# Kernel tuning notes

Hardware: AMD Instinct MI355X
Metric: run time of the kernel (lower is better)

The kernel has to match this reference:

```python
import jax, jax.numpy as jnp
import numpy as np

# Dimensions
B, T, S, V, CV, D = 32, 128, 400, 32000, 600, 512
PAD = 1  # vocabs['code'].stoi['<blank>']


def setup_inputs() -> dict:
    key = jax.random.key(0)
    k0, k1, k2, k3, k4 = jax.random.split(key, 5)
    hidden = jax.random.normal(k0, (B * T, D), dtype=jnp.float32)
    # attention weights: normalized over source length
    copy_attn = jax.nn.softmax(jax.random.normal(k1, (B * T, S), dtype=jnp.float32), axis=-1)
    # src_map: one-hot scatter matrix [B, S, CV] mapping src positions to extended-vocab ids
    src_ids = jax.random.randint(k2, (B, S), 0, CV)
    src_map = jax.nn.one_hot(src_ids, CV, dtype=jnp.float32)
    W = jax.random.normal(k3, (V, D), dtype=jnp.float32) * 0.02
    b = jnp.zeros((V,), dtype=jnp.float32)
    w_copy = jax.random.normal(k4, (D,), dtype=jnp.float32) * 0.02
    b_copy = jnp.zeros((), dtype=jnp.float32)
    return {"hidden": hidden, "copy_attn": copy_attn, "src_map": src_map,
            "W": W, "b": b, "w_copy": w_copy, "b_copy": b_copy}


def reference(hidden, copy_attn, src_map, W, b, w_copy, b_copy):
    # logits over target vocab, pad logit masked to -inf
    logits = hidden @ W.T + b                      # [B*T, V]
    logits = logits.at[:, PAD].set(-jnp.inf)
    prob = jax.nn.softmax(logits, axis=-1)         # [B*T, V]
    # copy gate p(z)
    copy = jax.nn.sigmoid(hidden @ w_copy + b_copy)[:, None]  # [B*T, 1]
    out_prob = prob * (1.0 - copy)                 # generation branch
    mul_attn = copy_attn * copy                    # copy branch, [B*T, S]
    # scatter attention mass into extended vocab via one-hot bmm
    copy_prob = jnp.einsum('bts,bsv->btv', mul_attn.reshape(B, T, S), src_map)
    copy_prob = copy_prob.reshape(-1, src_map.shape[-1])  # [B*T, CV]
    return jnp.concatenate([out_prob, copy_prob], axis=1)  # [B*T, V+CV]
```

## Files before the change

kernel.cpp:

```cpp
#include <hip/hip_runtime.h>
#include <hip/hip_bf16.h>
#include <hip/hip_fp8.h>
#include <cstdint>
#include <cstddef>

#define M_ROWS   4096
#define N_VOCAB  32000
#define K_DIM    512
#define S_DIM    400
#define CV_DIM   600
#define OUT_PITCH 32600
#define PAD_IDX  1

typedef __attribute__((ext_vector_type(8))) short short8;
typedef __attribute__((ext_vector_type(8))) unsigned short ushort8;
typedef __attribute__((ext_vector_type(4))) float f32x4;
typedef long long i64;

#define W8_OFF   0ull
#define H8_OFF   16384000ull
#define COPYG_OFF 18481152ull
#define RSUM_OFF  18497536ull
#define SSCALE_OFF 18513920ull
#define SRCID_OFF 18530304ull
#define EB_OFF    18581504ull
#define WS_NEED   (EB_OFF + 262144000ull)

__device__ inline void gload_lds16(const void* g, void* l) {
  __builtin_amdgcn_global_load_lds(
      (const __attribute__((address_space(1))) unsigned int*)g,
      (__attribute__((address_space(3))) unsigned int*)l, 16, 0, 0);
}

__device__ inline unsigned short f32_to_bf16_rn(float f) {
  unsigned u = __float_as_uint(f);
  u += 0x7FFFu + ((u >> 16) & 1u);
  return (unsigned short)(u >> 16);
}
__device__ inline float bf16_to_f32(unsigned short h) {
  return __uint_as_float((unsigned)h << 16);
}
__device__ inline unsigned f32_to_fp8(float f) {
  __hip_fp8_e4m3 q(f);
  return (unsigned)(unsigned char)q.__x;
}

__global__ void cvt8_kernel(const float4* __restrict__ in, unsigned* __restrict__ out, unsigned n4) {
  unsigned stride = gridDim.x * blockDim.x;
  for (unsigned i = blockIdx.x * blockDim.x + threadIdx.x; i < n4; i += stride) {
    float4 v = in[i];
    out[i] = f32_to_fp8(v.x) | (f32_to_fp8(v.y) << 8)
           | (f32_to_fp8(v.z) << 16) | (f32_to_fp8(v.w) << 24);
  }
}

__global__ void copygate_cvt_kernel(const float* __restrict__ hidden,
                                    const float* __restrict__ w_copy,
                                    const float* __restrict__ b_copy,
                                    float* __restrict__ copyg,
                                    unsigned char* __restrict__ H8) {
  unsigned gw = (blockIdx.x * blockDim.x + threadIdx.x) >> 6;
  unsigned lane = threadIdx.x & 63u;
  if (gw >= M_ROWS) return;
  const float4* h4 = (const float4*)(hidden + (size_t)gw * K_DIM);
  const float4* w4 = (const float4*)w_copy;
  float4 a0 = h4[lane * 2 + 0], w0 = w4[lane * 2 + 0];
  float4 a1 = h4[lane * 2 + 1], w1 = w4[lane * 2 + 1];
  float dot = a0.x * w0.x + a0.y * w0.y + a0.z * w0.z + a0.w * w0.w
            + a1.x * w1.x + a1.y * w1.y + a1.z * w1.z + a1.w * w1.w;
  unsigned lo = f32_to_fp8(a0.x) | (f32_to_fp8(a0.y) << 8)
              | (f32_to_fp8(a0.z) << 16) | (f32_to_fp8(a0.w) << 24);
  unsigned hi = f32_to_fp8(a1.x) | (f32_to_fp8(a1.y) << 8)
              | (f32_to_fp8(a1.z) << 16) | (f32_to_fp8(a1.w) << 24);
  uint2 pk; pk.x = lo; pk.y = hi;
  *(uint2*)(H8 + (size_t)gw * K_DIM + lane * 8u) = pk;
  #pragma unroll
  for (int mask = 1; mask < 64; mask <<= 1) dot += __shfl_xor(dot, mask);
  if (lane == 0) copyg[gw] = 1.f / (1.f + __expf(-(dot + b_copy[0])));
}

__global__ void srcids_kernel(const float* __restrict__ src_map, int* __restrict__ src_ids) {
  unsigned pos = (blockIdx.x * blockDim.x + threadIdx.x) >> 6;
  unsigned lane = threadIdx.x & 63u;
  if (pos >= 32 * S_DIM) return;
  const float* row = src_map + (size_t)pos * CV_DIM;
  int found = 1 << 30;
  for (int v = lane; v < CV_DIM; v += 64)
    if (row[v] > 0.5f) found = v;
  #pragma unroll
  for (int mask = 1; mask < 64; mask <<= 1) {
    int o = __shfl_xor(found, mask);
    found = found < o ? found : o;
  }
  if (lane == 0) src_ids[pos] = found;
}

template<int BF16OUT>
__global__ __launch_bounds__(512, 2)
void gemm_exp_kernel(const unsigned char* __restrict__ A,
                     const unsigned char* __restrict__ B,
                     const float* __restrict__ bias,
                     float* __restrict__ out,
                     unsigned short* __restrict__ Eb,
                     float* __restrict__ row_sum) {
  __shared__ unsigned char smem[49152];
  unsigned char* As = smem;
  unsigned char* Bs = smem + 32768;

  unsigned bid = blockIdx.x;
  unsigned xcd = bid & 7u, local = bid >> 3;
  unsigned slab = xcd >> 1, half = xcd & 1u;
  unsigned nt = half * 125u + (local >> 2);
  unsigned mt = slab * 4u + (local & 3u);
  unsigned m0 = mt * 256u, n0 = nt * 128u;

  unsigned tid = threadIdx.x;
  unsigned lane = tid & 63u;
  unsigned wid = tid >> 6;
  unsigned wm = wid >> 1, wn = wid & 1u;
  unsigned lr = lane >> 4, lc = lane & 15u;

  const unsigned char* Asrc[4];
  const unsigned char* Bsrc[2];
  unsigned dstA[4], dstB[2];
  #pragma unroll
  for (unsigned i = 0; i < 4; ++i) {
    unsigned u = i * 512u + tid;
    unsigned rr = u >> 3;
    unsigned ch = (u & 7u) ^ (rr & 7u);
    dstA[i] = u * 16u;
    Asrc[i] = A + (size_t)(m0 + rr) * K_DIM + ch * 16u;
  }
  #pragma unroll
  for (unsigned i = 0; i < 2; ++i) {
    unsigned u = i * 512u + tid;
    unsigned rr = u >> 3;
    unsigned ch = (u & 7u) ^ (rr & 7u);
    dstB[i] = u * 16u;
    Bsrc[i] = B + (size_t)(n0 + rr) * K_DIM + ch * 16u;
  }
  unsigned abase[4], akey[4], bbase[4], bkey[4];
  #pragma unroll
  for (int m = 0; m < 4; ++m) {
    unsigned r = wm * 64u + m * 16u + lc;
    abase[m] = r * 128u; akey[m] = r & 7u;
  }
  #pragma unroll
  for (int n = 0; n < 4; ++n) {
    unsigned r = wn * 64u + n * 16u + lc;
    bbase[n] = r * 128u; bkey[n] = r & 7u;
  }
  const unsigned hsel = (lr & 1u) * 8u;

  f32x4 acc[4][4] = {};

  for (unsigned kt = 0; kt < 4; ++kt) {
    unsigned k0 = kt * 128u;
    #pragma unroll
    for (unsigned i = 0; i < 4; ++i)
      gload_lds16(Asrc[i] + k0, As + dstA[i]);
    #pragma unroll
    for (unsigned i = 0; i < 2; ++i)
      gload_lds16(Bsrc[i] + k0, Bs + dstB[i]);
    __syncthreads();
    #pragma unroll
    for (unsigned ks = 0; ks < 4; ++ks) {
      unsigned h = ks * 2u + (lr >> 1);
      i64 av[4], bv[4];
      #pragma unroll
      for (int m = 0; m < 4; ++m)
        av[m] = *(const i64*)(As + abase[m] + ((h ^ akey[m]) * 16u) + hsel);
      #pragma unroll
      for (int n = 0; n < 4; ++n)
        bv[n] = *(const i64*)(Bs + bbase[n] + ((h ^ bkey[n]) * 16u) + hsel);
      #pragma unroll
      for (int m = 0; m < 4; ++m)
        #pragma unroll
        for (int n = 0; n < 4; ++n)
          acc[m][n] = __builtin_amdgcn_mfma_f32_16x16x32_fp8_fp8(bv[n], av[m],
                                                                 acc[m][n], 0, 0, 0);
    }
    __syncthreads();
  }

  float4 bv4[4];
  #pragma unroll
  for (int n = 0; n < 4; ++n)
    bv4[n] = *(const float4*)&bias[n0 + wn * 64u + n * 16u + lr * 4u];

  if (BF16OUT) {
    #pragma unroll
    for (int m = 0; m < 4; ++m) {
      unsigned grow = m0 + wm * 64u + m * 16u + lc;
      unsigned short* rowp = Eb + (size_t)grow * N_VOCAB;
      #pragma unroll
      for (int n = 0; n < 4; ++n) {
        unsigned gcol = n0 + wn * 64u + n * 16u + lr * 4u;
        float e0 = (gcol + 0u == PAD_IDX) ? 0.f : __expf(acc[m][n][0] + bv4[n].x);
        float e1 = (gcol + 1u == PAD_IDX) ? 0.f : __expf(acc[m][n][1] + bv4[n].y);
        float e2 = (gcol + 2u == PAD_IDX) ? 0.f : __expf(acc[m][n][2] + bv4[n].z);
        float e3 = (gcol + 3u == PAD_IDX) ? 0.f : __expf(acc[m][n][3] + bv4[n].w);
        ushort4 o;
        o.x = f32_to_bf16_rn(e0); o.y = f32_to_bf16_rn(e1);
        o.z = f32_to_bf16_rn(e2); o.w = f32_to_bf16_rn(e3);
        *(ushort4*)(rowp + gcol) = o;
      }
    }
  } else {
    #pragma unroll
    for (int m = 0; m < 4; ++m) {
      unsigned grow = m0 + wm * 64u + m * 16u + lc;
      float rs = 0.f;
      #pragma unroll
      for (int n = 0; n < 4; ++n) {
        unsigned gcol = n0 + wn * 64u + n * 16u + lr * 4u;
        float4 e;
        e.x = (gcol + 0u == PAD_IDX) ? 0.f : __expf(acc[m][n][0] + bv4[n].x);
        e.y = (gcol + 1u == PAD_IDX) ? 0.f : __expf(acc[m][n][1] + bv4[n].y);
        e.z = (gcol + 2u == PAD_IDX) ? 0.f : __expf(acc[m][n][2] + bv4[n].z);
        e.w = (gcol + 3u == PAD_IDX) ? 0.f : __expf(acc[m][n][3] + bv4[n].w);
        *(float4*)(out + (size_t)grow * OUT_PITCH + gcol) = e;
        rs += e.x + e.y + e.z + e.w;
      }
      rs += __shfl_xor(rs, 16);
      rs += __shfl_xor(rs, 32);
      if (lr == 0) atomicAdd(&row_sum[grow], rs);
    }
  }
}

__global__ __launch_bounds__(256)
void norm_scale_kernel(const unsigned short* __restrict__ Eb,
                       const float* __restrict__ copyg,
                       float* __restrict__ out) {
  unsigned r = blockIdx.x;
  unsigned tid = threadIdx.x;
  const ushort8* src = (const ushort8*)(Eb + (size_t)r * N_VOCAB);
  ushort8 v[16];
  float lsum = 0.f;
  #pragma unroll
  for (int i = 0; i < 16; ++i) {
    unsigned c = (unsigned)i * 256u + tid;
    if (c < 4000u) {
      v[i] = src[c];
      #pragma unroll
      for (int k = 0; k < 8; ++k) lsum += bf16_to_f32(v[i][k]);
    }
  }
  #pragma unroll
  for (int mask = 1; mask < 64; mask <<= 1) lsum += __shfl_xor(lsum, mask);
  __shared__ float wsum[4];
  if ((tid & 63u) == 0) wsum[tid >> 6] = lsum;
  __syncthreads();
  float s = (1.f - copyg[r]) / (wsum[0] + wsum[1] + wsum[2] + wsum[3]);
  float* dst = out + (size_t)r * OUT_PITCH;
  #pragma unroll
  for (int i = 0; i < 16; ++i) {
    unsigned c = (unsigned)i * 256u + tid;
    if (c < 4000u) {
      float4 lo, hi;
      lo.x = bf16_to_f32(v[i][0]) * s; lo.y = bf16_to_f32(v[i][1]) * s;
      lo.z = bf16_to_f32(v[i][2]) * s; lo.w = bf16_to_f32(v[i][3]) * s;
      hi.x = bf16_to_f32(v[i][4]) * s; hi.y = bf16_to_f32(v[i][5]) * s;
      hi.z = bf16_to_f32(v[i][6]) * s; hi.w = bf16_to_f32(v[i][7]) * s;
      float4* o = (float4*)(dst + c * 8u);
      o[0] = lo; o[1] = hi;
    }
  }
}

__global__ void finalize_kernel(const float* __restrict__ row_sum, const float* __restrict__ copyg,
                                float* __restrict__ sscale) {
  unsigned r = blockIdx.x * blockDim.x + threadIdx.x;
  if (r < M_ROWS) sscale[r] = (1.f - copyg[r]) / row_sum[r];
}

__global__ void scale_kernel(float4* __restrict__ out, const float* __restrict__ sscale) {
  const unsigned total = M_ROWS * (N_VOCAB / 4);
  unsigned stride = gridDim.x * blockDim.x;
  for (unsigned i = blockIdx.x * blockDim.x + threadIdx.x; i < total; i += stride) {
    unsigned r = i / (N_VOCAB / 4);
    unsigned c = i % (N_VOCAB / 4);
    float s = sscale[r];
    float4 v = out[(size_t)r * (OUT_PITCH / 4) + c];
    v.x *= s; v.y *= s; v.z *= s; v.w *= s;
    out[(size_t)r * (OUT_PITCH / 4) + c] = v;
  }
}

__global__ void copyprob_kernel(const float* __restrict__ attn, const int* __restrict__ src_ids,
                                const float* __restrict__ copyg, float* __restrict__ out) {
  unsigned r = blockIdx.x;
  unsigned tid = threadIdx.x;
  __shared__ float cp[CV_DIM];
  for (unsigned v = tid; v < CV_DIM; v += 128) cp[v] = 0.f;
  __syncthreads();
  unsigned batch = r >> 7;
  float g = copyg[r];
  for (unsigned s = tid; s < S_DIM; s += 128) {
    float a = attn[(size_t)r * S_DIM + s] * g;
    atomicAdd(&cp[src_ids[batch * S_DIM + s]], a);
  }
  __syncthreads();
  for (unsigned v = tid; v < CV_DIM; v += 128)
    out[(size_t)r * OUT_PITCH + N_VOCAB + v] = cp[v];
}

extern "C" void kernel_launch(void* const* d_in, const int* in_sizes, int n_in,
                              void* d_out, int out_size, void* d_ws, size_t ws_size,
                              hipStream_t stream) {
  const float* hidden    = (const float*)d_in[0];
  const float* copy_attn = (const float*)d_in[1];
  const float* src_map   = (const float*)d_in[2];
  const float* W         = (const float*)d_in[3];
  const float* bias      = (const float*)d_in[4];
  const float* w_copy    = (const float*)d_in[5];
  const float* b_copy    = (const float*)d_in[6];
  float* out = (float*)d_out;

  char* ws = (char*)d_ws;
  unsigned char* W8 = (unsigned char*)(ws + W8_OFF);
  unsigned char* H8 = (unsigned char*)(ws + H8_OFF);
  float* copyg   = (float*)(ws + COPYG_OFF);
  float* row_sum = (float*)(ws + RSUM_OFF);
  float* sscale  = (float*)(ws + SSCALE_OFF);
  int*   src_ids = (int*)(ws + SRCID_OFF);
  unsigned short* Eb = (unsigned short*)(ws + EB_OFF);

  const bool bf16_path = (ws_size >= WS_NEED);

  cvt8_kernel<<<2048, 256, 0, stream>>>((const float4*)W, (unsigned*)W8,
                                        (unsigned)(N_VOCAB * K_DIM / 4));
  copygate_cvt_kernel<<<M_ROWS / 4, 256, 0, stream>>>(hidden, w_copy, b_copy, copyg, H8);
  srcids_kernel<<<(32 * S_DIM) / 4, 256, 0, stream>>>(src_map, src_ids);

  if (bf16_path) {
    gemm_exp_kernel<1><<<(M_ROWS / 256) * (N_VOCAB / 128), 512, 0, stream>>>(
        H8, W8, bias, out, Eb, row_sum);
    norm_scale_kernel<<<M_ROWS, 256, 0, stream>>>(Eb, copyg, out);
  } else {
    hipMemsetAsync(row_sum, 0, M_ROWS * sizeof(float), stream);
    gemm_exp_kernel<0><<<(M_ROWS / 256) * (N_VOCAB / 128), 512, 0, stream>>>(
        H8, W8, bias, out, Eb, row_sum);
    finalize_kernel<<<(M_ROWS + 255) / 256, 256, 0, stream>>>(row_sum, copyg, sscale);
    scale_kernel<<<4096, 256, 0, stream>>>((float4*)out, sscale);
  }

  copyprob_kernel<<<M_ROWS, 128, 0, stream>>>(copy_attn, src_ids, copyg, out);
}
```

Measured before the change: 363.5 us.

## Double-buffer GEMM K-tiles and fuse copy-prob scatter into normalize kernel

The fp8 GEMM now uses 64-wide K tiles in two LDS buffers and prefetches the next tile while computing the current one, aiming to hide global-load latency. The copy-probability scatter is folded into the normalize/scale kernel using shared-memory atomics, removing a separate launch on the bf16 path. Smaller K tiles mean more iterations and barriers, and the synchronization around buffer reuse must be correct to avoid races.

```diff
diff --git a/kernel.cpp b/kernel.cpp
--- a/kernel.cpp
+++ b/kernel.cpp
@@ -104,8 +104,6 @@
                      unsigned short* __restrict__ Eb,
                      float* __restrict__ row_sum) {
   __shared__ unsigned char smem[49152];
-  unsigned char* As = smem;
-  unsigned char* Bs = smem + 32768;
 
   unsigned bid = blockIdx.x;
   unsigned xcd = bid & 7u, local = bid >> 3;
@@ -120,59 +118,67 @@
   unsigned wm = wid >> 1, wn = wid & 1u;
   unsigned lr = lane >> 4, lc = lane & 15u;
 
-  const unsigned char* Asrc[4];
-  const unsigned char* Bsrc[2];
-  unsigned dstA[4], dstB[2];
-  #pragma unroll
-  for (unsigned i = 0; i < 4; ++i) {
+  const unsigned char* Asrc[2];
+  const unsigned char* Bsrc0;
+  unsigned dstA[2], dstB0;
+  #pragma unroll
+  for (unsigned i = 0; i < 2; ++i) {
     unsigned u = i * 512u + tid;
-    unsigned rr = u >> 3;
-    unsigned ch = (u & 7u) ^ (rr & 7u);
+    unsigned rr = u >> 2;
+    unsigned ch = (u & 3u) ^ (rr & 3u);
     dstA[i] = u * 16u;
     Asrc[i] = A + (size_t)(m0 + rr) * K_DIM + ch * 16u;
   }
-  #pragma unroll
-  for (unsigned i = 0; i < 2; ++i) {
-    unsigned u = i * 512u + tid;
-    unsigned rr = u >> 3;
-    unsigned ch = (u & 7u) ^ (rr & 7u);
-    dstB[i] = u * 16u;
-    Bsrc[i] = B + (size_t)(n0 + rr) * K_DIM + ch * 16u;
+  {
+    unsigned u = tid;
+    unsigned rr = u >> 2;
+    unsigned ch = (u & 3u) ^ (rr & 3u);
+    dstB0 = u * 16u;
+    Bsrc0 = B + (size_t)(n0 + rr) * K_DIM + ch * 16u;
   }
   unsigned abase[4], akey[4], bbase[4], bkey[4];
   #pragma unroll
   for (int m = 0; m < 4; ++m) {
     unsigned r = wm * 64u + m * 16u + lc;
-    abase[m] = r * 128u; akey[m] = r & 7u;
+    abase[m] = r * 64u; akey[m] = r & 3u;
   }
   #pragma unroll
   for (int n = 0; n < 4; ++n) {
     unsigned r = wn * 64u + n * 16u + lc;
-    bbase[n] = r * 128u; bkey[n] = r & 7u;
+    bbase[n] = 16384u + r * 64u; bkey[n] = r & 3u;
   }
   const unsigned hsel = (lr & 1u) * 8u;
 
   f32x4 acc[4][4] = {};
 
-  for (unsigned kt = 0; kt < 4; ++kt) {
-    unsigned k0 = kt * 128u;
+  {
+    unsigned char* base = smem;
+    gload_lds16(Asrc[0], base + dstA[0]);
+    gload_lds16(Asrc[1], base + dstA[1]);
+    gload_lds16(Bsrc0, base + 16384u + dstB0);
+  }
+  __syncthreads();
+
+  for (unsigned kt = 0; kt < 8; ++kt) {
+    unsigned buf = kt & 1u;
+    if (kt < 7) {
+      unsigned k0 = (kt + 1u) * 64u;
+      unsigned char* base = smem + (buf ^ 1u) * 24576u;
+      gload_lds16(Asrc[0] + k0, base + dstA[0]);
+      gload_lds16(Asrc[1] + k0, base + dstA[1]);
+      gload_lds16(Bsrc0 + k0, base + 16384u + dstB0);
+    }
+    const unsigned char* cbase = smem + buf * 24576u;
     #pragma unroll
-    for (unsigned i = 0; i < 4; ++i)
-      gload_lds16(Asrc[i] + k0, As + dstA[i]);
-    #pragma unroll
-    for (unsigned i = 0; i < 2; ++i)
-      gload_lds16(Bsrc[i] + k0, Bs + dstB[i]);
-    __syncthreads();
-    #pragma unroll
-    for (unsigned ks = 0; ks < 4; ++ks) {
+    for (unsigned ks = 0; ks < 2; ++ks) {
       unsigned h = ks * 2u + (lr >> 1);
       i64 av[4], bv[4];
       #pragma unroll
       for (int m = 0; m < 4; ++m)
-        av[m] = *(const i64*)(As + abase[m] + ((h ^ akey[m]) * 16u) + hsel);
+        av[m] = *(const i64*)(cbase + abase[m] + ((h ^ akey[m]) * 16u) + hsel);
       #pragma unroll
       for (int n = 0; n < 4; ++n)
-        bv[n] = *(const i64*)(Bs + bbase[n] + ((h ^ bkey[n]) * 16u) + hsel);
+        bv[n] = *(const i64*)(cbase + bbase[n] + ((h ^ bkey[n]) * 16u) + hsel);
       #pragma unroll
       for (int m = 0; m < 4; ++m)
         #pragma unroll
@@ -230,11 +236,17 @@
 }
 
 __global__ __launch_bounds__(256)
-void norm_scale_kernel(const unsigned short* __restrict__ Eb,
-                       const float* __restrict__ copyg,
-                       float* __restrict__ out) {
+void norm_scale_copy_kernel(const unsigned short* __restrict__ Eb,
+                            const float* __restrict__ copyg,
+                            const float* __restrict__ attn,
+                            const int* __restrict__ src_ids,
+                            float* __restrict__ out) {
   unsigned r = blockIdx.x;
   unsigned tid = threadIdx.x;
+  __shared__ float cp[CV_DIM];
+  __shared__ float wsum[4];
+  for (unsigned v2 = tid; v2 < CV_DIM; v2 += 256) cp[v2] = 0.f;
+
   const ushort8* src = (const ushort8*)(Eb + (size_t)r * N_VOCAB);
   ushort8 v[16];
   float lsum = 0.f;
@@ -249,10 +261,18 @@
   }
   #pragma unroll
   for (int mask = 1; mask < 64; mask <<= 1) lsum += __shfl_xor(lsum, mask);
-  __shared__ float wsum[4];
   if ((tid & 63u) == 0) wsum[tid >> 6] = lsum;
   __syncthreads();
-  float s = (1.f - copyg[r]) / (wsum[0] + wsum[1] + wsum[2] + wsum[3]);
+
+  float g = copyg[r];
+  float s = (1.f - g) / (wsum[0] + wsum[1] + wsum[2] + wsum[3]);
+
+  unsigned batch = r >> 7;
+  for (unsigned sp = tid; sp < S_DIM; sp += 256) {
+    float a = attn[(size_t)r * S_DIM + sp] * g;
+    atomicAdd(&cp[src_ids[batch * S_DIM + sp]], a);
+  }
+
   float* dst = out + (size_t)r * OUT_PITCH;
   #pragma unroll
   for (int i = 0; i < 16; ++i) {
@@ -267,6 +287,9 @@
       o[0] = lo; o[1] = hi;
     }
   }
+  __syncthreads();
+  for (unsigned v2 = tid; v2 < CV_DIM; v2 += 256)
+    dst[N_VOCAB + v2] = cp[v2];
 }
 
 __global__ void finalize_kernel(const float* __restrict__ row_sum, const float* __restrict__ copyg,
@@ -337,14 +360,13 @@
   if (bf16_path) {
     gemm_exp_kernel<1><<<(M_ROWS / 256) * (N_VOCAB / 128), 512, 0, stream>>>(
         H8, W8, bias, out, Eb, row_sum);
-    norm_scale_kernel<<<M_ROWS, 256, 0, stream>>>(Eb, copyg, out);
+    norm_scale_copy_kernel<<<M_ROWS, 256, 0, stream>>>(Eb, copyg, copy_attn, src_ids, out);
   } else {
     hipMemsetAsync(row_sum, 0, M_ROWS * sizeof(float), stream);
     gemm_exp_kernel<0><<<(M_ROWS / 256) * (N_VOCAB / 128), 512, 0, stream>>>(
         H8, W8, bias, out, Eb, row_sum);
     finalize_kernel<<<(M_ROWS + 255) / 256, 256, 0, stream>>>(row_sum, copyg, sscale);
     scale_kernel<<<4096, 256, 0, stream>>>((float4*)out, sscale);
-  }
-
-  copyprob_kernel<<<M_ROWS, 128, 0, stream>>>(copy_attn, src_ids, copyg, out);
-}
+    copyprob_kernel<<<M_ROWS, 128, 0, stream>>>(copy_attn, src_ids, copyg, out);
+  }
+}
```

New measurement: 398.6 us. 9.6% more time.
